# Optimization experiments

Hardware: AMD Instinct MI355X
Metric: run time of the kernel (lower is better)

Reference implementation:

```python
import jax, jax.numpy as jnp
import numpy as np
import math

D_MODEL = 1024
N_HEADS = 16
BATCH = 2
SEQ = 2048

def setup_inputs() -> dict:
    key = jax.random.key(0)
    ks = jax.random.split(key, 5)
    d = D_MODEL
    lim_qkv = 1.0 / math.sqrt(d)
    x = jax.random.normal(ks[0], (BATCH, SEQ, d), dtype=jnp.float32)
    qkv_w = jax.random.uniform(ks[1], (3 * d, d), dtype=jnp.float32, minval=-lim_qkv, maxval=lim_qkv)
    qkv_b = jax.random.uniform(ks[2], (3 * d,), dtype=jnp.float32, minval=-lim_qkv, maxval=lim_qkv)
    out_w = jax.random.uniform(ks[3], (d, d), dtype=jnp.float32, minval=-lim_qkv, maxval=lim_qkv)
    out_b = jax.random.uniform(ks[4], (d,), dtype=jnp.float32, minval=-lim_qkv, maxval=lim_qkv)
    return {"x": x, "qkv_w": qkv_w, "qkv_b": qkv_b, "out_w": out_w, "out_b": out_b}

def reference(x, qkv_w, qkv_b, out_w, out_b):
    b, s, d = x.shape
    h = N_HEADS
    hd = d // h
    # note: original uses float division for scale: sqrt(in_features / n_heads)
    scale = math.sqrt(d / h)
    qkv = x @ qkv_w.T + qkv_b                      # [b, s, 3d]
    q, k, v = jnp.split(qkv, 3, axis=-1)           # each [b, s, d]
    def heads(t):
        return t.reshape(b, s, h, hd).transpose(0, 2, 1, 3)  # [b, h, s, hd]
    qh, kh, vh = heads(q), heads(k), heads(v)
    # faithful quirk: scores = k @ q^T (k as query, q as key)
    scores = jnp.einsum('bhid,bhjd->bhij', kh, qh) / scale   # [b, h, s, s]
    alpha = jax.nn.softmax(scores, axis=-1)
    attn = jnp.einsum('bhij,bhjd->bhid', alpha, vh)          # [b, h, s, hd]
    attn = attn.transpose(0, 2, 1, 3).reshape(b, s, d)       # [b, s, d]
    return attn @ out_w.T + out_b
```

## Files before the change

kernel.cpp:

```cpp
#include <hip/hip_runtime.h>
#include <hip/hip_fp16.h>

#define D_MODEL 1024
#define N_HEADS 16
#define HEAD_DIM 64
#define BATCH 2
#define SEQ 2048
#define ROWS (BATCH*SEQ)

#define K_SCALE 0.18033688011112042f

using h8v = __attribute__((ext_vector_type(8))) _Float16;
using h4v = __attribute__((ext_vector_type(4))) _Float16;
using g2v = __attribute__((ext_vector_type(2))) __fp16;
using g4v = __attribute__((ext_vector_type(4))) __fp16;
using f4v = __attribute__((ext_vector_type(4))) float;

__device__ __forceinline__ ushort f2h_u(float x) { return __half_as_ushort(__float2half(x)); }
__device__ __forceinline__ void splith(float x, ushort& h, ushort& l) {
    __half hh_ = __float2half(x);
    h = __half_as_ushort(hh_);
    l = f2h_u(x - __half2float(hh_));
}

__device__ __forceinline__ size_t fidx(int row, int k) {
    return ((size_t)((row >> 7) * 32 + (k >> 5)) << 12)
         + (size_t)(((row & 127) >> 4) << 9)
         + (size_t)(((row & 15) * 4 + ((k & 31) >> 3)) << 3) + (k & 7);
}

__device__ __forceinline__ void async_lds16(const ushort* g, ushort* l) {
    __builtin_amdgcn_global_load_lds(
        (const __attribute__((address_space(1))) unsigned int*)g,
        (__attribute__((address_space(3))) unsigned int*)l, 16, 0, 0);
}

__global__ __launch_bounds__(256)
void prep_kernel(const float* __restrict__ x, const float* __restrict__ qw,
                 const float* __restrict__ ow,
                 ushort* __restrict__ xh, ushort* __restrict__ qwh,
                 ushort* __restrict__ owh, ushort* __restrict__ owl)
{
    const int b = blockIdx.x, t = threadIdx.x;
    if (b < 4096) {
        const int i = b * 256 + t;
        const int row = i >> 8, k4 = (i & 255) * 4;
        const float4 v = ((const float4*)x)[i];
        ushort4 h;
        h.x = f2h_u(v.x); h.y = f2h_u(v.y); h.z = f2h_u(v.z); h.w = f2h_u(v.w);
        *(ushort4*)&xh[fidx(row, k4)] = h;
    } else if (b < 7168) {
        const int i = (b - 4096) * 256 + t;
        const int row = i >> 8, k4 = (i & 255) * 4;
        const float4 v = ((const float4*)qw)[i];
        ushort4 h;
        h.x = f2h_u(v.x); h.y = f2h_u(v.y); h.z = f2h_u(v.z); h.w = f2h_u(v.w);
        *(ushort4*)&qwh[fidx(row, k4)] = h;
    } else {
        const int i = (b - 7168) * 256 + t;
        const int row = i >> 8, k4 = (i & 255) * 4;
        const float4 v = ((const float4*)ow)[i];
        const size_t o = fidx(row, k4);
        ushort4 h, l;
        splith(v.x, h.x, l.x); splith(v.y, h.y, l.y);
        splith(v.z, h.z, l.z); splith(v.w, h.w, l.w);
        *(ushort4*)&owh[o] = h; *(ushort4*)&owl[o] = l;
    }
}

__global__ __launch_bounds__(256, 5)
void gemm_qkv(const ushort* __restrict__ Af, const ushort* __restrict__ Wf,
              const float* __restrict__ bias,
              ushort* __restrict__ Qh, ushort* __restrict__ Kh,
              ushort* __restrict__ Vt)
{
    __shared__ ushort sA[2][4096], sW[2][2048];
    const int t = threadIdx.x, lane = t & 63, wv = t >> 6;
    const int tx = lane & 15, g = lane >> 4;
    const int lin = blockIdx.x;
    const int xcd = lin & 7, r = lin >> 3;
    const int mb = xcd * 4 + (r & 3);
    const int nb = r >> 2;
    const int at0 = (wv >> 1) * 4, wt0 = (wv & 1) * 2;
    const int fo = (tx * 4 + g) * 8;
    const size_t wbase = ((size_t)(nb & 1)) << 11;

    f4v acc[8];
#pragma unroll
    for (int i = 0; i < 8; i++)
#pragma unroll
        for (int e = 0; e < 4; e++) acc[i][e] = 0.f;

    {
        const size_t ao = ((size_t)(mb * 32)) << 12;
        const size_t wo = (((size_t)((nb >> 1) * 32)) << 12) + wbase;
#pragma unroll
        for (int c = 0; c < 2; c++) {
            const int o = (t + c * 256) * 8;
            async_lds16(Af + ao + o, &sA[0][o]);
        }
        async_lds16(Wf + wo + t * 8, &sW[0][t * 8]);
    }

    for (int kt = 0; kt < 32; kt++) {
        const int p = kt & 1;
        __syncthreads();
        if (kt < 31) {
            const size_t ao = ((size_t)(mb * 32 + kt + 1)) << 12;
            const size_t wo = (((size_t)((nb >> 1) * 32 + kt + 1)) << 12) + wbase;
#pragma unroll
            for (int c = 0; c < 2; c++) {
                const int o = (t + c * 256) * 8;
                async_lds16(Af + ao + o, &sA[p ^ 1][o]);
            }
            async_lds16(Wf + wo + t * 8, &sW[p ^ 1][t * 8]);
        }
        h8v ah[4], wh[2];
#pragma unroll
        for (int i = 0; i < 4; i++)
            ah[i] = *(const h8v*)&sA[p][(at0 + i) * 512 + fo];
#pragma unroll
        for (int i = 0; i < 2; i++)
            wh[i] = *(const h8v*)&sW[p][(wt0 + i) * 512 + fo];
        if (nb < 32) {
#pragma unroll
            for (int wi = 0; wi < 2; wi++)
#pragma unroll
                for (int ai = 0; ai < 4; ai++)
                    acc[wi * 4 + ai] = __builtin_amdgcn_mfma_f32_16x16x32_f16(wh[wi], ah[ai], acc[wi * 4 + ai], 0, 0, 0);
        } else {
#pragma unroll
            for (int ai = 0; ai < 4; ai++)
#pragma unroll
                for (int wi = 0; wi < 2; wi++)
                    acc[ai * 2 + wi] = __builtin_amdgcn_mfma_f32_16x16x32_f16(ah[ai], wh[wi], acc[ai * 2 + wi], 0, 0, 0);
        }
    }

    if (nb < 32) {
        const int part = nb >> 4;
        ushort* dst = part ? Kh : Qh;
        const float scale = part ? K_SCALE : 1.0f;
#pragma unroll
        for (int wi = 0; wi < 2; wi++) {
            const int gf0 = nb * 64 + (wv & 1) * 32 + wi * 16 + g * 4;
            const float4 bv = *(const float4*)&bias[gf0];
            const int gfl = gf0 & 1023;
            const int hh = gfl >> 6;
            const int dd = gfl & 63;
#pragma unroll
            for (int ai = 0; ai < 4; ai++) {
                const int s = mb * 128 + (wv >> 1) * 64 + ai * 16 + tx;
                const int bb = s >> 11, srel = s & 2047;
                const size_t idx = (size_t)(bb * N_HEADS + hh) * 131072
                    + (size_t)(srel >> 4) * 1024 + (size_t)(dd >> 5) * 512
                    + ((srel & 15) * 4 + ((dd & 31) >> 3)) * 8 + (dd & 7);
                const f4v a = acc[wi * 4 + ai];
                ushort4 h4;
                h4.x = f2h_u((a[0] + bv.x) * scale);
                h4.y = f2h_u((a[1] + bv.y) * scale);
                h4.z = f2h_u((a[2] + bv.z) * scale);
                h4.w = f2h_u((a[3] + bv.w) * scale);
                *(ushort4*)&dst[idx] = h4;
            }
        }
    } else {
#pragma unroll
        for (int wi = 0; wi < 2; wi++) {
            const int gf = nb * 64 + (wv & 1) * 32 + wi * 16 + tx;
            const float bv = bias[gf];
            const int gfl = gf & 1023;
            const int hh = gfl >> 6;
            const int dl = gfl & 63;
#pragma unroll
            for (int ai = 0; ai < 4; ai++) {
                const int jt0 = mb * 128 + (wv >> 1) * 64 + ai * 16 + g * 4;
                const int bb = jt0 >> 11, jr = jt0 & 2047;
                const size_t idx = (size_t)(bb * N_HEADS + hh) * 131072
                    + (size_t)(jr >> 6) * 4096
                    + (size_t)((((jr >> 4) & 3) * 4) + (dl >> 4)) * 256
                    + (((jr >> 2) & 3) * 16 + (dl & 15)) * 4;
                const f4v a = acc[ai * 2 + wi];
                ushort4 h4;
                h4.x = f2h_u(a[0] + bv);
                h4.y = f2h_u(a[1] + bv);
                h4.z = f2h_u(a[2] + bv);
                h4.w = f2h_u(a[3] + bv);
                *(ushort4*)&Vt[idx] = h4;
            }
        }
    }
}

__global__ __launch_bounds__(256)
void attn_mfma(const ushort* __restrict__ Kf, const ushort* __restrict__ Qf,
               const ushort* __restrict__ Vf,
               ushort* __restrict__ Oh, ushort* __restrict__ Ol)
{
    __shared__ ushort lds[16384];
    ushort* K0 = lds + 8192;

    const int t = threadIdx.x, lane = t & 63, wv = t >> 6;
    const int tx = lane & 15, g = lane >> 4;
    const int lin = blockIdx.x;
    const int xcd = lin & 7, ix = lin >> 3;
    const int bh = xcd * 4 + (ix >> 5);
    const int it = ix & 31;
    const int b = bh >> 4, h = bh & 15;
    const int i0 = it * 64;
    const size_t hb = (size_t)bh * 131072;

    {
        const size_t kb = hb + (size_t)it * 4096;
#pragma unroll
        for (int c = 0; c < 2; c++) {
            const int o = (t + c * 256) * 8;
            async_lds16(Kf + kb + o, K0 + o);
            async_lds16(Qf + hb + o, lds + o);
            async_lds16(Vf + hb + o, lds + 4096 + o);
        }
    }
    __syncthreads();

    const int fo = (tx * 4 + g) * 8;
    h8v kf[2];
#pragma unroll
    for (int kk = 0; kk < 2; kk++)
        kf[kk] = *(const h8v*)&K0[(wv * 2 + kk) * 512 + fo];

    f4v O[4];
    float l_acc = 0.f;
#pragma unroll
    for (int ht = 0; ht < 4; ht++)
#pragma unroll
        for (int e = 0; e < 4; e++) O[ht][e] = 0.f;

    for (int jt = 0; jt < SEQ / 64; jt++) {
        ushort* buf = lds + (jt & 1) * 8192;
        ushort* nxt = lds + ((jt & 1) ^ 1) * 8192;
        __syncthreads();
        if (jt < SEQ / 64 - 1) {
            const size_t off = hb + (size_t)(jt + 1) * 4096;
#pragma unroll
            for (int c = 0; c < 2; c++) {
                const int o = (t + c * 256) * 8;
                async_lds16(Qf + off + o, nxt + o);
                async_lds16(Vf + off + o, nxt + 4096 + o);
            }
        }
        const ushort* sQ = buf;
        const ushort* sV = buf + 4096;

        f4v sc[4];
#pragma unroll
        for (int jn = 0; jn < 4; jn++)
#pragma unroll
            for (int e = 0; e < 4; e++) sc[jn][e] = 0.f;
#pragma unroll
        for (int kk = 0; kk < 2; kk++)
#pragma unroll
            for (int jn = 0; jn < 4; jn++) {
                const h8v qf = *(const h8v*)&sQ[(jn * 2 + kk) * 512 + fo];
                sc[jn] = __builtin_amdgcn_mfma_f32_16x16x32_f16(qf, kf[kk], sc[jn], 0, 0, 0);
            }

        h4v ph[4];
#pragma unroll
        for (int jn = 0; jn < 4; jn++) {
            const float p0 = __builtin_amdgcn_exp2f(sc[jn][0]);
            const float p1 = __builtin_amdgcn_exp2f(sc[jn][1]);
            const float p2 = __builtin_amdgcn_exp2f(sc[jn][2]);
            const float p3 = __builtin_amdgcn_exp2f(sc[jn][3]);
            l_acc += (p0 + p1) + (p2 + p3);
            const g2v plo = __builtin_amdgcn_cvt_pkrtz(p0, p1);
            const g2v phi = __builtin_amdgcn_cvt_pkrtz(p2, p3);
            const g4v pk = __builtin_shufflevector(plo, phi, 0, 1, 2, 3);
            ph[jn] = __builtin_bit_cast(h4v, pk);
        }

#pragma unroll
        for (int jc = 0; jc < 4; jc++)
#pragma unroll
            for (int ht = 0; ht < 4; ht++) {
                const h4v vf = *(const h4v*)&sV[(jc * 4 + ht) * 256 + (g * 16 + tx) * 4];
                O[ht] = __builtin_amdgcn_mfma_f32_16x16x16f16(vf, ph[jc], O[ht], 0, 0, 0);
            }
    }

    {
        float l = l_acc;
        l += __shfl_xor(l, 16);
        l += __shfl_xor(l, 32);
        const float inv = 1.0f / l;
        const int row = b * SEQ + i0 + wv * 16 + tx;
#pragma unroll
        for (int ht = 0; ht < 4; ht++) {
            const int k0 = h * 64 + ht * 16 + g * 4;
            const size_t o = fidx(row, k0);
            ushort4 hv, lv;
            float v;
            v = O[ht][0] * inv; splith(v, hv.x, lv.x);
            v = O[ht][1] * inv; splith(v, hv.y, lv.y);
            v = O[ht][2] * inv; splith(v, hv.z, lv.z);
            v = O[ht][3] * inv; splith(v, hv.w, lv.w);
            *(ushort4*)&Oh[o] = hv;
            *(ushort4*)&Ol[o] = lv;
        }
    }
}

__global__ __launch_bounds__(256, 4)
void gemm_out(const ushort* __restrict__ Af, const ushort* __restrict__ Alf,
              const ushort* __restrict__ Wf, const ushort* __restrict__ Wlf,
              const float* __restrict__ bias, float* __restrict__ out)
{
    __shared__ ushort sA[2][4096], sW[2][4096];
    const int t = threadIdx.x, lane = t & 63, wv = t >> 6;
    const int tx = lane & 15, g = lane >> 4;
    const int lin = blockIdx.x;
    const int xcd = lin & 7, r = lin >> 3;
    const int nb = xcd * 2 + (r & 1);
    const int mb = r >> 1;
    const int at0 = (wv >> 1) * 2, wt0 = (wv & 1) * 2;
    const int fo = (tx * 4 + g) * 8;
    const size_t abase = ((size_t)(mb & 1)) << 11;
    const size_t wbase = ((size_t)(nb & 1)) << 11;

    f4v acc[4];
#pragma unroll
    for (int i = 0; i < 4; i++)
#pragma unroll
        for (int e = 0; e < 4; e++) acc[i][e] = 0.f;

    {
        const size_t ao = (((size_t)((mb >> 1) * 32)) << 12) + abase;
        const size_t wo = (((size_t)((nb >> 1) * 32)) << 12) + wbase;
        const int o = t * 8;
        async_lds16(Af + ao + o, &sA[0][o]);
        async_lds16(Alf + ao + o, &sA[0][2048 + o]);
        async_lds16(Wf + wo + o, &sW[0][o]);
        async_lds16(Wlf + wo + o, &sW[0][2048 + o]);
    }

    for (int kt = 0; kt < 32; kt++) {
        const int p = kt & 1;
        __syncthreads();
        if (kt < 31) {
            const size_t ao = (((size_t)((mb >> 1) * 32 + kt + 1)) << 12) + abase;
            const size_t wo = (((size_t)((nb >> 1) * 32 + kt + 1)) << 12) + wbase;
            const int o = t * 8;
            async_lds16(Af + ao + o, &sA[p ^ 1][o]);
            async_lds16(Alf + ao + o, &sA[p ^ 1][2048 + o]);
            async_lds16(Wf + wo + o, &sW[p ^ 1][o]);
            async_lds16(Wlf + wo + o, &sW[p ^ 1][2048 + o]);
        }
        h8v ah[2], al[2], wh[2], wl[2];
#pragma unroll
        for (int i = 0; i < 2; i++) {
            ah[i] = *(const h8v*)&sA[p][(at0 + i) * 512 + fo];
            al[i] = *(const h8v*)&sA[p][2048 + (at0 + i) * 512 + fo];
            wh[i] = *(const h8v*)&sW[p][(wt0 + i) * 512 + fo];
            wl[i] = *(const h8v*)&sW[p][2048 + (wt0 + i) * 512 + fo];
        }
#pragma unroll
        for (int wi = 0; wi < 2; wi++)
#pragma unroll
            for (int ai = 0; ai < 2; ai++) {
                acc[wi * 2 + ai] = __builtin_amdgcn_mfma_f32_16x16x32_f16(wh[wi], ah[ai], acc[wi * 2 + ai], 0, 0, 0);
                acc[wi * 2 + ai] = __builtin_amdgcn_mfma_f32_16x16x32_f16(wh[wi], al[ai], acc[wi * 2 + ai], 0, 0, 0);
                acc[wi * 2 + ai] = __builtin_amdgcn_mfma_f32_16x16x32_f16(wl[wi], ah[ai], acc[wi * 2 + ai], 0, 0, 0);
            }
    }

#pragma unroll
    for (int wi = 0; wi < 2; wi++) {
        const int gf0 = nb * 64 + (wv & 1) * 32 + wi * 16 + g * 4;
        const float4 bv = *(const float4*)&bias[gf0];
#pragma unroll
        for (int ai = 0; ai < 2; ai++) {
            const int tok = mb * 64 + (wv >> 1) * 32 + ai * 16 + tx;
            const f4v a = acc[wi * 2 + ai];
            float4 o;
            o.x = a[0] + bv.x;
            o.y = a[1] + bv.y;
            o.z = a[2] + bv.z;
            o.w = a[3] + bv.w;
            *(float4*)&out[(size_t)tok * D_MODEL + gf0] = o;
        }
    }
}

extern "C" void kernel_launch(void* const* d_in, const int* in_sizes, int n_in,
                              void* d_out, int out_size, void* d_ws, size_t ws_size,
                              hipStream_t stream) {
    const float* x     = (const float*)d_in[0];
    const float* qkv_w = (const float*)d_in[1];
    const float* qkv_b = (const float*)d_in[2];
    const float* out_w = (const float*)d_in[3];
    const float* out_b = (const float*)d_in[4];
    float* out = (float*)d_out;

    const size_t FB = (size_t)ROWS * D_MODEL;
    const size_t MM = (size_t)D_MODEL * D_MODEL;
    ushort* u   = (ushort*)d_ws;
    ushort* xh  = u;
    ushort* Ol  = u + FB;
    ushort* Qh  = u + 2 * FB;
    ushort* Kh  = u + 3 * FB;
    ushort* Vt  = u + 4 * FB;
    ushort* qwh = u + 5 * FB;
    ushort* owh = u + 5 * FB + 3 * MM;
    ushort* owl = owh + MM;

    prep_kernel<<<8192, 256, 0, stream>>>(x, qkv_w, out_w, xh, qwh, owh, owl);
    gemm_qkv<<<1536, 256, 0, stream>>>(xh, qwh, qkv_b, Qh, Kh, Vt);
    attn_mfma<<<1024, 256, 0, stream>>>(Kh, Qh, Vt, xh, Ol);
    gemm_out<<<1024, 256, 0, stream>>>(xh, Ol, owh, owl, out_b, out);
}
```

Before: 220.1 us.

## Process two 16-row query strips per wave in attention to reuse Q/V fragments

Each attention block now covers 128 rows instead of 64, with every wave handling two 16-row strips that share each LDS-loaded Q and V fragment across two MFMA chains. This halves LDS read traffic and global Q/V streaming per output row, and the grid is halved to match. In exchange it doubles accumulator registers per wave and halves the number of blocks, which may reduce occupancy and the ability to hide latency.

After: 215.4 us. -2.1%, faster.

```diff
diff --git a/kernel.cpp b/kernel.cpp
--- a/kernel.cpp
+++ b/kernel.cpp
@@ -204,18 +204,22 @@
     const int tx = lane & 15, g = lane >> 4;
     const int lin = blockIdx.x;
     const int xcd = lin & 7, ix = lin >> 3;
-    const int bh = xcd * 4 + (ix >> 5);
-    const int it = ix & 31;
+    const int bh = xcd * 4 + (ix >> 4);
+    const int it = ix & 15;
     const int b = bh >> 4, h = bh & 15;
-    const int i0 = it * 64;
+    const int i0 = it * 128;
     const size_t hb = (size_t)bh * 131072;
 
     {
-        const size_t kb = hb + (size_t)it * 4096;
+        const size_t kb = hb + (size_t)it * 8192;
+#pragma unroll
+        for (int c = 0; c < 4; c++) {
+            const int o = (t + c * 256) * 8;
+            async_lds16(Kf + kb + o, K0 + o);
+        }
 #pragma unroll
         for (int c = 0; c < 2; c++) {
             const int o = (t + c * 256) * 8;
-            async_lds16(Kf + kb + o, K0 + o);
             async_lds16(Qf + hb + o, lds + o);
             async_lds16(Vf + hb + o, lds + 4096 + o);
         }
@@ -223,17 +227,21 @@
     __syncthreads();
 
     const int fo = (tx * 4 + g) * 8;
-    h8v kf[2];
-#pragma unroll
-    for (int kk = 0; kk < 2; kk++)
-        kf[kk] = *(const h8v*)&K0[(wv * 2 + kk) * 512 + fo];
-
-    f4v O[4];
-    float l_acc = 0.f;
-#pragma unroll
-    for (int ht = 0; ht < 4; ht++)
-#pragma unroll
-        for (int e = 0; e < 4; e++) O[ht][e] = 0.f;
+    h8v kf[2][2];
+#pragma unroll
+    for (int is = 0; is < 2; is++)
+#pragma unroll
+        for (int kk = 0; kk < 2; kk++)
+            kf[is][kk] = *(const h8v*)&K0[((wv * 2 + is) * 2 + kk) * 512 + fo];
+
+    f4v O[2][4];
+    float l_acc[2] = {0.f, 0.f};
+#pragma unroll
+    for (int is = 0; is < 2; is++)
+#pragma unroll
+        for (int ht = 0; ht < 4; ht++)
+#pragma unroll
+            for (int e = 0; e < 4; e++) O[is][ht][e] = 0.f;
 
     for (int jt = 0; jt < SEQ / 64; jt++) {
         ushort* buf = lds + (jt & 1) * 8192;
@@ -251,58 +259,67 @@
         const ushort* sQ = buf;
         const ushort* sV = buf + 4096;
 
-        f4v sc[4];
-#pragma unroll
-        for (int jn = 0; jn < 4; jn++)
-#pragma unroll
-            for (int e = 0; e < 4; e++) sc[jn][e] = 0.f;
+        f4v sc[2][4];
+#pragma unroll
+        for (int is = 0; is < 2; is++)
+#pragma unroll
+            for (int jn = 0; jn < 4; jn++)
+#pragma unroll
+                for (int e = 0; e < 4; e++) sc[is][jn][e] = 0.f;
 #pragma unroll
         for (int kk = 0; kk < 2; kk++)
 #pragma unroll
             for (int jn = 0; jn < 4; jn++) {
                 const h8v qf = *(const h8v*)&sQ[(jn * 2 + kk) * 512 + fo];
-                sc[jn] = __builtin_amdgcn_mfma_f32_16x16x32_f16(qf, kf[kk], sc[jn], 0, 0, 0);
-            }
-
-        h4v ph[4];
-#pragma unroll
-        for (int jn = 0; jn < 4; jn++) {
-            const float p0 = __builtin_amdgcn_exp2f(sc[jn][0]);
-            const float p1 = __builtin_amdgcn_exp2f(sc[jn][1]);
-            const float p2 = __builtin_amdgcn_exp2f(sc[jn][2]);
-            const float p3 = __builtin_amdgcn_exp2f(sc[jn][3]);
-            l_acc += (p0 + p1) + (p2 + p3);
-            const g2v plo = __builtin_amdgcn_cvt_pkrtz(p0, p1);
-            const g2v phi = __builtin_amdgcn_cvt_pkrtz(p2, p3);
-            const g4v pk = __builtin_shufflevector(plo, phi, 0, 1, 2, 3);
-            ph[jn] = __builtin_bit_cast(h4v, pk);
-        }
+#pragma unroll
+                for (int is = 0; is < 2; is++)
+                    sc[is][jn] = __builtin_amdgcn_mfma_f32_16x16x32_f16(qf, kf[is][kk], sc[is][jn], 0, 0, 0);
+            }
+
+        h4v ph[2][4];
+#pragma unroll
+        for (int is = 0; is < 2; is++)
+#pragma unroll
+            for (int jn = 0; jn < 4; jn++) {
+                const float p0 = __builtin_amdgcn_exp2f(sc[is][jn][0]);
+                const float p1 = __builtin_amdgcn_exp2f(sc[is][jn][1]);
+                const float p2 = __builtin_amdgcn_exp2f(sc[is][jn][2]);
+                const float p3 = __builtin_amdgcn_exp2f(sc[is][jn][3]);
+                l_acc[is] += (p0 + p1) + (p2 + p3);
+                const g2v plo = __builtin_amdgcn_cvt_pkrtz(p0, p1);
+                const g2v phi = __builtin_amdgcn_cvt_pkrtz(p2, p3);
+                const g4v pk = __builtin_shufflevector(plo, phi, 0, 1, 2, 3);
+                ph[is][jn] = __builtin_bit_cast(h4v, pk);
+            }
 
 #pragma unroll
         for (int jc = 0; jc < 4; jc++)
 #pragma unroll
             for (int ht = 0; ht < 4; ht++) {
                 const h4v vf = *(const h4v*)&sV[(jc * 4 + ht) * 256 + (g * 16 + tx) * 4];
-                O[ht] = __builtin_amdgcn_mfma_f32_16x16x16f16(vf, ph[jc], O[ht], 0, 0, 0);
-            }
-    }
-
-    {
-        float l = l_acc;
+#pragma unroll
+                for (int is = 0; is < 2; is++)
+                    O[is][ht] = __builtin_amdgcn_mfma_f32_16x16x16f16(vf, ph[is][jc], O[is][ht], 0, 0, 0);
+            }
+    }
+
+#pragma unroll
+    for (int is = 0; is < 2; is++) {
+        float l = l_acc[is];
         l += __shfl_xor(l, 16);
         l += __shfl_xor(l, 32);
         const float inv = 1.0f / l;
-        const int row = b * SEQ + i0 + wv * 16 + tx;
+        const int row = b * SEQ + i0 + (wv * 2 + is) * 16 + tx;
 #pragma unroll
         for (int ht = 0; ht < 4; ht++) {
             const int k0 = h * 64 + ht * 16 + g * 4;
             const size_t o = fidx(row, k0);
             ushort4 hv, lv;
             float v;
-            v = O[ht][0] * inv; splith(v, hv.x, lv.x);
-            v = O[ht][1] * inv; splith(v, hv.y, lv.y);
-            v = O[ht][2] * inv; splith(v, hv.z, lv.z);
-            v = O[ht][3] * inv; splith(v, hv.w, lv.w);
+            v = O[is][ht][0] * inv; splith(v, hv.x, lv.x);
+            v = O[is][ht][1] * inv; splith(v, hv.y, lv.y);
+            v = O[is][ht][2] * inv; splith(v, hv.z, lv.z);
+            v = O[is][ht][3] * inv; splith(v, hv.w, lv.w);
             *(ushort4*)&Oh[o] = hv;
             *(ushort4*)&Ol[o] = lv;
         }
@@ -414,6 +431,6 @@
 
     prep_kernel<<<8192, 256, 0, stream>>>(x, qkv_w, out_w, xh, qwh, owh, owl);
     gemm_qkv<<<1536, 256, 0, stream>>>(xh, qwh, qkv_b, Qh, Kh, Vt);
-    attn_mfma<<<1024, 256, 0, stream>>>(Kh, Qh, Vt, xh, Ol);
+    attn_mfma<<<512, 256, 0, stream>>>(Kh, Qh, Vt, xh, Ol);
     gemm_out<<<1024, 256, 0, stream>>>(xh, Ol, owh, owl, out_b, out);
 }
```
